# Performance work log

Hardware: AMD Instinct MI355X
Metric: run time of the kernel (lower is better)

## Reference

```python
import jax, jax.numpy as jnp
import numpy as np

QMAX = 127.0

def quantize_mat(mat):
    # per-row (last-dim) absmax scale, kept in fp16 like the torch code,
    # truncating cast to int8 (XLA float->int convert truncates toward zero, same as torch .to(int8))
    max_val = (jnp.max(jnp.abs(mat), axis=-1) / QMAX).astype(jnp.float16)
    q = (mat / max_val[..., None]).astype(jnp.int8)
    return q, max_val


def setup_inputs() -> dict:
    key = jax.random.key(0)
    k1, k2, k3, k4 = jax.random.split(key, 4)
    B, S, IN, OUT = 8, 4096, 2048, 2048
    x = jax.random.normal(k1, (B, S, IN), dtype=jnp.float16)
    ori_w = jax.random.normal(k2, (OUT, IN), dtype=jnp.float16)
    # SmoothQuant scales: positive, bounded away from 0 (torch clamps min=1e-5)
    scales = (jax.random.uniform(k3, (IN,), dtype=jnp.float16) + jnp.float16(0.5))
    bias = jax.random.normal(k4, (OUT,), dtype=jnp.float16)
    return {"x": x, "ori_w": ori_w, "scales": scales, "bias": bias}


def reference(x, ori_w, scales, bias):
    dtype = x.dtype
    # __init__-time: smooth the weight then quantize per output row
    w = (ori_w * scales).astype(dtype)                 # [OUT, IN]
    weight_q, w_max = quantize_mat(w)                  # int8 [OUT, IN], fp16 [OUT]
    weight_qt = weight_q.T                             # stored transposed [IN, OUT]
    # forward: smooth + quantize activations
    x = (x / scales).astype(dtype)                     # [B, S, IN]
    x_q, x_max = quantize_mat(x)                       # int8 [B,S,IN], fp16 [B,S]
    res_q = jnp.matmul(x_q.astype(jnp.float32), weight_qt.astype(jnp.float32))  # [B,S,OUT]
    # dequant factor: outer product of activation and weight scales (fp16 linear, then fp32)
    mx = (x_max[..., None] * w_max).astype(jnp.float32)  # [B,S,OUT]
    res = (res_q * mx).astype(dtype)
    res = res + bias
    return res
```

## Files before the change

kernel.cpp:

```cpp
#include <hip/hip_runtime.h>
#include <hip/hip_bf16.h>
#include <cstdint>
#include <cstddef>

#define M_TOT 32768
#define N_OUT 2048
#define K_IN  2048

typedef int v4i __attribute__((ext_vector_type(4)));

__device__ __forceinline__ void gload16(const int8_t* g, int8_t* l) {
  __builtin_amdgcn_global_load_lds(
      (const __attribute__((address_space(1))) void*)g,
      (__attribute__((address_space(3))) void*)l, 16, 0, 0);
}

__global__ __launch_bounds__(256) void quant_rows_kernel(
    const float* __restrict__ in,
    const float* __restrict__ scales,
    int8_t* __restrict__ q, float* __restrict__ rmax, int mul_mode)
{
  const int row = blockIdx.x;
  const int tid = threadIdx.x;
  const size_t base = (size_t)row * K_IN + tid * 8;
  const float4 xv0 = *(const float4*)(in + base);
  const float4 xv1 = *(const float4*)(in + base + 4);
  const float4 sv0 = *(const float4*)(scales + tid * 8);
  const float4 sv1 = *(const float4*)(scales + tid * 8 + 4);
  const float xf[8] = {xv0.x, xv0.y, xv0.z, xv0.w, xv1.x, xv1.y, xv1.z, xv1.w};
  const float sf[8] = {sv0.x, sv0.y, sv0.z, sv0.w, sv1.x, sv1.y, sv1.z, sv1.w};
  _Float16 xs[8];
  float amax = 0.f;
#pragma unroll
  for (int i = 0; i < 8; ++i) {
    const _Float16 hx = (_Float16)xf[i];
    const _Float16 hs = (_Float16)sf[i];
    xs[i] = mul_mode ? (_Float16)(hx * hs) : (_Float16)(hx / hs);
    amax = fmaxf(amax, fabsf((float)xs[i]));
  }
#pragma unroll
  for (int off = 32; off; off >>= 1) amax = fmaxf(amax, __shfl_down(amax, off));
  __shared__ float red[4];
  const int wid = tid >> 6, lane = tid & 63;
  if (lane == 0) red[wid] = amax;
  __syncthreads();
  amax = fmaxf(fmaxf(red[0], red[1]), fmaxf(red[2], red[3]));
  _Float16 hqm = (_Float16)amax / (_Float16)127.0f;
  if (tid == 0) rmax[row] = (float)hqm;
  if (hqm == (_Float16)0.f) hqm = (_Float16)1.0f;
  int8_t qb[8];
#pragma unroll
  for (int i = 0; i < 8; ++i) {
    const float qf = (float)(_Float16)(xs[i] / hqm);
    qb[i] = (int8_t)(int)qf;
  }
  unsigned long long pk;
  __builtin_memcpy(&pk, qb, 8);
  *(unsigned long long*)(q + (size_t)row * K_IN + tid * 8) = pk;
}

__global__ __launch_bounds__(512, 2) void gemm_i8_kernel(
    const int8_t* __restrict__ Aq, const int8_t* __restrict__ Bq,
    const float* __restrict__ Am, const float* __restrict__ Bm,
    const float* __restrict__ bias, float* __restrict__ out)
{
  __shared__ __align__(16) int8_t lds[8 * 16384];
  const int tid = threadIdx.x;
  const int w = tid >> 6, lane = tid & 63;
  const int wm = w >> 2, wn = w & 3;
  const int bx = blockIdx.x & 7;
  const int by = blockIdx.x >> 3;
  const long bm = (long)by * 256;
  const int  bn = bx * 256;

  const int schunk = ((lane & 3) ^ ((lane >> 3) & 3)) * 16;
  const int srow = w * 16 + (lane >> 2);
  const int8_t* gA = Aq + (bm + srow) * (long)K_IN + schunk;
  const int8_t* gB = Bq + ((long)(bn + srow)) * K_IN + schunk;

  const int fr = lane & 15, fq = lane >> 4;
  const int pc = (fq ^ ((fr >> 1) & 3)) * 16;
  const int aoff = (wm * 128 + fr) * 64 + pc;
  const int boff = (wn * 64  + fr) * 64 + pc;

  v4i acc[8][4] = {};
  v4i bfr[4];

#define STAGE(G) do {                                                         \
    const int g_ = (G);                                                       \
    const long koff_ = (long)((g_ >> 2) * 128 + ((g_ >> 1) & 1) * 64);        \
    int8_t* const ld_ = lds + (g_ & 7) * 16384 + w * 1024;                    \
    const int8_t* const gp_ = (g_ & 1) ? gB : gA;                             \
    gload16(gp_ + koff_,                  ld_);                               \
    gload16(gp_ + koff_ + 128L * K_IN,    ld_ + 8192);                        \
  } while (0)

#define VMCNT(N) asm volatile("s_waitcnt vmcnt(" #N ")" ::: "memory")
#define BAR() do { asm volatile("" ::: "memory");                             \
                   __builtin_amdgcn_s_barrier();                              \
                   asm volatile("" ::: "memory"); } while (0)

#define QUAD(T, KH, MH) do {                                                  \
    const int sa_ = (((T) & 1) * 4 + (KH) * 2) * 16384;                       \
    if ((MH) == 0) {                                                          \
      _Pragma("unroll")                                                       \
      for (int ni = 0; ni < 4; ++ni)                                          \
        bfr[ni] = *(const v4i*)(lds + sa_ + 16384 + boff + ni * 1024);        \
    }                                                                         \
    v4i afr[4];                                                               \
    _Pragma("unroll")                                                         \
    for (int mi = 0; mi < 4; ++mi)                                            \
      afr[mi] = *(const v4i*)(lds + sa_ + aoff + ((MH) * 64 + mi * 16) * 64); \
    __builtin_amdgcn_s_setprio(1);                                            \
    _Pragma("unroll")                                                         \
    for (int mi = 0; mi < 4; ++mi)                                            \
      _Pragma("unroll")                                                       \
      for (int ni = 0; ni < 4; ++ni)                                          \
        acc[(MH) * 4 + mi][ni] = __builtin_amdgcn_mfma_i32_16x16x64_i8(       \
            afr[mi], bfr[ni], acc[(MH) * 4 + mi][ni], 0, 0, 0);               \
    __builtin_amdgcn_s_setprio(0);                                            \
  } while (0)

  STAGE(0); STAGE(1); STAGE(2); STAGE(3);
  STAGE(4); VMCNT(8); BAR();

#pragma unroll 2
  for (int t = 0; t < 14; ++t) {
    STAGE(4 * t + 5); VMCNT(8); BAR(); QUAD(t, 0, 0);
    STAGE(4 * t + 6); VMCNT(8); BAR(); QUAD(t, 0, 1);
    STAGE(4 * t + 7); VMCNT(8); BAR(); QUAD(t, 1, 0);
    STAGE(4 * t + 8); VMCNT(8); BAR(); QUAD(t, 1, 1);
  }
  STAGE(61); VMCNT(8); BAR(); QUAD(14, 0, 0);
  STAGE(62); VMCNT(8); BAR(); QUAD(14, 0, 1);
  STAGE(63); VMCNT(8); BAR(); QUAD(14, 1, 0);
  VMCNT(0);  BAR();
  QUAD(14, 1, 1);
  QUAD(15, 0, 0); QUAD(15, 0, 1); QUAD(15, 1, 0); QUAD(15, 1, 1);

#undef STAGE
#undef VMCNT
#undef BAR
#undef QUAD

  const long cm0 = bm + wm * 128;
  const int  cn0 = bn + wn * 64;
  float amv[8][4];
#pragma unroll
  for (int mi = 0; mi < 8; ++mi)
#pragma unroll
    for (int r = 0; r < 4; ++r)
      amv[mi][r] = Am[cm0 + mi * 16 + fq * 4 + r];
#pragma unroll
  for (int ni = 0; ni < 4; ++ni) {
    const int col = cn0 + ni * 16 + fr;
    const float wmv = Bm[col];
    const _Float16 bsv = (_Float16)bias[col];
#pragma unroll
    for (int mi = 0; mi < 8; ++mi) {
#pragma unroll
      for (int r = 0; r < 4; ++r) {
        const long row = cm0 + mi * 16 + fq * 4 + r;
        const float mx = (float)(_Float16)((_Float16)amv[mi][r] * (_Float16)wmv);
        const _Float16 resh = (_Float16)((float)acc[mi][ni][r] * mx);
        out[row * N_OUT + col] = (float)(_Float16)(resh + bsv);
      }
    }
  }
}

extern "C" void kernel_launch(void* const* d_in, const int* in_sizes, int n_in,
                              void* d_out, int out_size, void* d_ws, size_t ws_size,
                              hipStream_t stream) {
  const float* x      = (const float*)d_in[0];
  const float* ori_w  = (const float*)d_in[1];
  const float* scales = (const float*)d_in[2];
  const float* bias   = (const float*)d_in[3];
  float* out = (float*)d_out;

  int8_t* xq = (int8_t*)d_ws;
  int8_t* wq = xq + (size_t)M_TOT * K_IN;
  float*  xm = (float*)(wq + (size_t)N_OUT * K_IN);
  float*  wmx = xm + M_TOT;

  quant_rows_kernel<<<M_TOT, 256, 0, stream>>>(x, scales, xq, xm, 0);
  quant_rows_kernel<<<N_OUT, 256, 0, stream>>>(ori_w, scales, wq, wmx, 1);

  gemm_i8_kernel<<<dim3(1024), 512, 0, stream>>>(xq, wq, xm, wmx, bias, out);
}
```

Baseline: 593.0 us.

## Wave-per-row quantization, deeper GEMM prefetch with split LDS reads, nontemporal I/O

Result: no change. 587.8 us (-0.9%).

```diff
diff --git a/kernel.cpp b/kernel.cpp
--- a/kernel.cpp
+++ b/kernel.cpp
@@ -7,7 +7,8 @@
 #define N_OUT 2048
 #define K_IN  2048
 
-typedef int v4i __attribute__((ext_vector_type(4)));
+typedef int   v4i __attribute__((ext_vector_type(4)));
+typedef float v4f __attribute__((ext_vector_type(4)));
 
 __device__ __forceinline__ void gload16(const int8_t* g, int8_t* l) {
   __builtin_amdgcn_global_load_lds(
@@ -15,48 +16,49 @@
       (__attribute__((address_space(3))) void*)l, 16, 0, 0);
 }
 
-__global__ __launch_bounds__(256) void quant_rows_kernel(
+__global__ __launch_bounds__(256) void quant_rows_wave(
     const float* __restrict__ in,
     const float* __restrict__ scales,
-    int8_t* __restrict__ q, float* __restrict__ rmax, int mul_mode)
+    int8_t* __restrict__ q, float* __restrict__ rmax,
+    int nrows, int mul_mode)
 {
-  const int row = blockIdx.x;
-  const int tid = threadIdx.x;
-  const size_t base = (size_t)row * K_IN + tid * 8;
-  const float4 xv0 = *(const float4*)(in + base);
-  const float4 xv1 = *(const float4*)(in + base + 4);
-  const float4 sv0 = *(const float4*)(scales + tid * 8);
-  const float4 sv1 = *(const float4*)(scales + tid * 8 + 4);
-  const float xf[8] = {xv0.x, xv0.y, xv0.z, xv0.w, xv1.x, xv1.y, xv1.z, xv1.w};
-  const float sf[8] = {sv0.x, sv0.y, sv0.z, sv0.w, sv1.x, sv1.y, sv1.z, sv1.w};
-  _Float16 xs[8];
-  float amax = 0.f;
+  const int wib = threadIdx.x >> 6, lane = threadIdx.x & 63;
+  for (int row = blockIdx.x * 4 + wib; row < nrows; row += gridDim.x * 4) {
+    const float* rp = in + (size_t)row * K_IN;
+    _Float16 xs[32];
+    float amax = 0.f;
 #pragma unroll
-  for (int i = 0; i < 8; ++i) {
-    const _Float16 hx = (_Float16)xf[i];
-    const _Float16 hs = (_Float16)sf[i];
-    xs[i] = mul_mode ? (_Float16)(hx * hs) : (_Float16)(hx / hs);
-    amax = fmaxf(amax, fabsf((float)xs[i]));
+    for (int c = 0; c < 8; ++c) {
+      const int off = c * 256 + lane * 4;
+      const v4f xv = __builtin_nontemporal_load((const v4f*)(rp + off));
+      const v4f sv = *(const v4f*)(scales + off);
+#pragma unroll
+      for (int j = 0; j < 4; ++j) {
+        const _Float16 hx = (_Float16)xv[j];
+        const _Float16 hs = (_Float16)sv[j];
+        const _Float16 v = mul_mode ? (_Float16)(hx * hs) : (_Float16)(hx / hs);
+        xs[c * 4 + j] = v;
+        amax = fmaxf(amax, fabsf((float)v));
+      }
+    }
+#pragma unroll
+    for (int off = 32; off; off >>= 1) amax = fmaxf(amax, __shfl_xor(amax, off));
+    _Float16 hqm = (_Float16)amax / (_Float16)127.0f;
+    if (lane == 0) rmax[row] = (float)hqm;
+    if (hqm == (_Float16)0.f) hqm = (_Float16)1.0f;
+#pragma unroll
+    for (int c = 0; c < 8; ++c) {
+      int8_t qb[4];
+#pragma unroll
+      for (int j = 0; j < 4; ++j) {
+        const float qf = (float)(_Float16)(xs[c * 4 + j] / hqm);
+        qb[j] = (int8_t)(int)qf;
+      }
+      int pk;
+      __builtin_memcpy(&pk, qb, 4);
+      *(int*)(q + (size_t)row * K_IN + c * 256 + lane * 4) = pk;
+    }
   }
-#pragma unroll
-  for (int off = 32; off; off >>= 1) amax = fmaxf(amax, __shfl_down(amax, off));
-  __shared__ float red[4];
-  const int wid = tid >> 6, lane = tid & 63;
-  if (lane == 0) red[wid] = amax;
-  __syncthreads();
-  amax = fmaxf(fmaxf(red[0], red[1]), fmaxf(red[2], red[3]));
-  _Float16 hqm = (_Float16)amax / (_Float16)127.0f;
-  if (tid == 0) rmax[row] = (float)hqm;
-  if (hqm == (_Float16)0.f) hqm = (_Float16)1.0f;
-  int8_t qb[8];
-#pragma unroll
-  for (int i = 0; i < 8; ++i) {
-    const float qf = (float)(_Float16)(xs[i] / hqm);
-    qb[i] = (int8_t)(int)qf;
-  }
-  unsigned long long pk;
-  __builtin_memcpy(&pk, qb, 8);
-  *(unsigned long long*)(q + (size_t)row * K_IN + tid * 8) = pk;
 }
 
 __global__ __launch_bounds__(512, 2) void gemm_i8_kernel(
@@ -84,7 +86,7 @@
   const int boff = (wn * 64  + fr) * 64 + pc;
 
   v4i acc[8][4] = {};
-  v4i bfr[4];
+  v4i afr[4], bfr[4];
 
 #define STAGE(G) do {                                                         \
     const int g_ = (G);                                                       \
@@ -100,17 +102,19 @@
                    __builtin_amdgcn_s_barrier();                              \
                    asm volatile("" ::: "memory"); } while (0)
 
-#define QUAD(T, KH, MH) do {                                                  \
+#define READS(T, KH, MH) do {                                                 \
     const int sa_ = (((T) & 1) * 4 + (KH) * 2) * 16384;                       \
     if ((MH) == 0) {                                                          \
       _Pragma("unroll")                                                       \
       for (int ni = 0; ni < 4; ++ni)                                          \
         bfr[ni] = *(const v4i*)(lds + sa_ + 16384 + boff + ni * 1024);        \
     }                                                                         \
-    v4i afr[4];                                                               \
     _Pragma("unroll")                                                         \
     for (int mi = 0; mi < 4; ++mi)                                            \
       afr[mi] = *(const v4i*)(lds + sa_ + aoff + ((MH) * 64 + mi * 16) * 64); \
+  } while (0)
+
+#define MFMA16(MH) do {                                                       \
     __builtin_amdgcn_s_setprio(1);                                            \
     _Pragma("unroll")                                                         \
     for (int mi = 0; mi < 4; ++mi)                                            \
@@ -121,27 +125,30 @@
     __builtin_amdgcn_s_setprio(0);                                            \
   } while (0)
 
-  STAGE(0); STAGE(1); STAGE(2); STAGE(3);
-  STAGE(4); VMCNT(8); BAR();
+  STAGE(0); STAGE(1); STAGE(2); STAGE(3); STAGE(4); STAGE(5);
+  VMCNT(8); BAR();
 
 #pragma unroll 2
   for (int t = 0; t < 14; ++t) {
-    STAGE(4 * t + 5); VMCNT(8); BAR(); QUAD(t, 0, 0);
-    STAGE(4 * t + 6); VMCNT(8); BAR(); QUAD(t, 0, 1);
-    STAGE(4 * t + 7); VMCNT(8); BAR(); QUAD(t, 1, 0);
-    STAGE(4 * t + 8); VMCNT(8); BAR(); QUAD(t, 1, 1);
+    READS(t, 0, 0); STAGE(4 * t + 6); VMCNT(8); BAR(); MFMA16(0); BAR();
+    READS(t, 0, 1); STAGE(4 * t + 7); VMCNT(8); BAR(); MFMA16(1); BAR();
+    READS(t, 1, 0); STAGE(4 * t + 8); VMCNT(8); BAR(); MFMA16(0); BAR();
+    READS(t, 1, 1); STAGE(4 * t + 9); VMCNT(8); BAR(); MFMA16(1); BAR();
   }
-  STAGE(61); VMCNT(8); BAR(); QUAD(14, 0, 0);
-  STAGE(62); VMCNT(8); BAR(); QUAD(14, 0, 1);
-  STAGE(63); VMCNT(8); BAR(); QUAD(14, 1, 0);
-  VMCNT(0);  BAR();
-  QUAD(14, 1, 1);
-  QUAD(15, 0, 0); QUAD(15, 0, 1); QUAD(15, 1, 0); QUAD(15, 1, 1);
+  READS(14, 0, 0); STAGE(62); VMCNT(8); BAR(); MFMA16(0); BAR();
+  READS(14, 0, 1); STAGE(63); VMCNT(8); BAR(); MFMA16(1); BAR();
+  READS(14, 1, 0);             BAR(); MFMA16(0); BAR();
+  READS(14, 1, 1); VMCNT(4);   BAR(); MFMA16(1); BAR();
+  READS(15, 0, 0);                              BAR(); MFMA16(0); BAR();
+  READS(15, 0, 1); VMCNT(0);   BAR(); MFMA16(1); BAR();
+  READS(15, 1, 0); MFMA16(0);
+  READS(15, 1, 1); MFMA16(1);
 
 #undef STAGE
 #undef VMCNT
 #undef BAR
-#undef QUAD
+#undef READS
+#undef MFMA16
 
   const long cm0 = bm + wm * 128;
   const int  cn0 = bn + wn * 64;
@@ -163,7 +170,8 @@
         const long row = cm0 + mi * 16 + fq * 4 + r;
         const float mx = (float)(_Float16)((_Float16)amv[mi][r] * (_Float16)wmv);
         const _Float16 resh = (_Float16)((float)acc[mi][ni][r] * mx);
-        out[row * N_OUT + col] = (float)(_Float16)(resh + bsv);
+        __builtin_nontemporal_store((float)(_Float16)(resh + bsv),
+                                    out + row * N_OUT + col);
       }
     }
   }
@@ -183,8 +191,8 @@
   float*  xm = (float*)(wq + (size_t)N_OUT * K_IN);
   float*  wmx = xm + M_TOT;
 
-  quant_rows_kernel<<<M_TOT, 256, 0, stream>>>(x, scales, xq, xm, 0);
-  quant_rows_kernel<<<N_OUT, 256, 0, stream>>>(ori_w, scales, wq, wmx, 1);
+  quant_rows_wave<<<2048, 256, 0, stream>>>(x, scales, xq, xm, M_TOT, 0);
+  quant_rows_wave<<<512,  256, 0, stream>>>(ori_w, scales, wq, wmx, N_OUT, 1);
 
   gemm_i8_kernel<<<dim3(1024), 512, 0, stream>>>(xq, wq, xm, wmx, bias, out);
 }
```
